# Kernel optimization log

Measured on AMD Instinct MI355X. Metric: run time of the kernel, lower is better.

## Reference

```python
import jax, jax.numpy as jnp
import numpy as np

NEG = -1e9  # additive mask value for padded keys


def layer_norm(x, g, b, eps=1e-5):
    m = x.mean(-1, keepdims=True)
    v = ((x - m) ** 2).mean(-1, keepdims=True)
    return (x - m) / jnp.sqrt(v + eps) * g + b


def setup_inputs() -> dict:
    key = jax.random.key(0)
    G, n, H, heads, L, F, De, deg = 64, 256, 256, 8, 4, 512, 16, 32
    N = G * n
    E = N * deg
    ks = jax.random.split(key, 24)
    s = 0.02
    node_embs = jax.random.normal(ks[0], (N, H), jnp.float32)
    batch_vec = jnp.arange(N, dtype=jnp.int32) // n          # [N] sorted graph ids
    ptr = jnp.arange(G + 1, dtype=jnp.int32) * n              # [G+1]
    epg = E // G
    g_idx = jnp.repeat(jnp.arange(G, dtype=jnp.int32), epg)
    src = g_idx * n + jax.random.randint(ks[1], (E,), 0, n)
    dst = g_idx * n + jax.random.randint(ks[2], (E,), 0, n)
    edge_index = jnp.stack([src, dst])                        # [2,E] intra-graph edges
    edge_attr = jax.random.normal(ks[3], (E, De), jnp.float32)
    return {
        "node_embs": node_embs, "batch_vec": batch_vec, "ptr": ptr,
        "edge_index": edge_index, "edge_attr": edge_attr,
        "edge_proj_w": jax.random.normal(ks[4], (heads, De), jnp.float32) * s,
        "edge_proj_b": jnp.zeros((heads,), jnp.float32),
        "Wqkv": jax.random.normal(ks[5], (L, 3 * H, H), jnp.float32) * s,
        "bqkv": jnp.zeros((L, 3 * H), jnp.float32),
        "Wo": jax.random.normal(ks[6], (L, H, H), jnp.float32) * s,
        "bo": jnp.zeros((L, H), jnp.float32),
        "ln1_g": jnp.ones((L, H), jnp.float32), "ln1_b": jnp.zeros((L, H), jnp.float32),
        "ln2_g": jnp.ones((L, H), jnp.float32), "ln2_b": jnp.zeros((L, H), jnp.float32),
        "W1": jax.random.normal(ks[7], (L, F, H), jnp.float32) * s,
        "b1": jnp.zeros((L, F), jnp.float32),
        "W2": jax.random.normal(ks[8], (L, H, F), jnp.float32) * s,
        "b2": jnp.zeros((L, H), jnp.float32),
        "norm_g": jnp.ones((H,), jnp.float32), "norm_b": jnp.zeros((H,), jnp.float32),
    }


def reference(node_embs, batch_vec, ptr, edge_index, edge_attr,
              edge_proj_w, edge_proj_b, Wqkv, bqkv, Wo, bo,
              ln1_g, ln1_b, ln2_g, ln2_b, W1, b1, W2, b2, norm_g, norm_b):
    N, H = node_embs.shape
    G = ptr.shape[0] - 1
    maxN = N // G  # graphs are equal-sized -> static max_N
    L = Wqkv.shape[0]
    heads = edge_proj_w.shape[0]
    dh = H // heads

    # to_dense_batch: scatter nodes into [G, maxN, H] with validity mask
    local = jnp.arange(N) - ptr[batch_vec]
    dense = jnp.zeros((G, maxN, H), node_embs.dtype).at[batch_vec, local].set(node_embs)
    valid = jnp.zeros((G, maxN), bool).at[batch_vec, local].set(True)

    # scatter-add per-head edge bias -> [G, heads, maxN, maxN]
    src, dst = edge_index[0], edge_index[1]
    g = batch_vec[src]
    sl = src - ptr[g]
    dl = dst - ptr[g]
    ea = edge_attr @ edge_proj_w.T + edge_proj_b  # [E, heads]
    bias = jnp.zeros((G, maxN, maxN, heads), ea.dtype).at[g, sl, dl].add(ea)
    bias = bias.transpose(0, 3, 1, 2)

    pad = jnp.where(valid, 0.0, NEG)[:, None, None, :]  # [G,1,1,maxN] key padding
    mask = bias + pad
    scale = 1.0 / np.sqrt(dh)

    x = dense
    for i in range(L):  # pre-norm TransformerEncoderLayer (relu activation)
        y = layer_norm(x, ln1_g[i], ln1_b[i])
        qkv = y @ Wqkv[i].T + bqkv[i]
        q, k, v = jnp.split(qkv, 3, -1)
        q = q.reshape(G, maxN, heads, dh).transpose(0, 2, 1, 3)
        k = k.reshape(G, maxN, heads, dh).transpose(0, 2, 1, 3)
        v = v.reshape(G, maxN, heads, dh).transpose(0, 2, 1, 3)
        scores = jnp.einsum('ghqd,ghkd->ghqk', q, k) * scale + mask
        p = jax.nn.softmax(scores, axis=-1)
        o = jnp.einsum('ghqk,ghkd->ghqd', p, v).transpose(0, 2, 1, 3).reshape(G, maxN, H)
        x = x + o @ Wo[i].T + bo[i]
        y2 = layer_norm(x, ln2_g[i], ln2_b[i])
        x = x + jax.nn.relu(y2 @ W1[i].T + b1[i]) @ W2[i].T + b2[i]

    out = layer_norm(x, norm_g, norm_b)
    return (out * valid[..., None]).sum(axis=1)  # [G, H] sum-pool over valid nodes
```

## Files before the change

kernel.cpp:

```cpp
#include <hip/hip_runtime.h>
#include <hip/hip_bf16.h>

#define GG   64
#define NPG  256
#define NN   16384
#define HH   256
#define HEADS 8
#define DH   32
#define LAYERS 4
#define FF   512
#define DE   16
#define NE   524288
#define EPG  8192
#define ECAP 160

typedef __attribute__((ext_vector_type(8))) short bf16x8_t;
typedef __attribute__((ext_vector_type(4))) short s16x4;
typedef __attribute__((ext_vector_type(4))) float f32x4;
typedef __attribute__((ext_vector_type(4))) unsigned int u32x4;

typedef const __attribute__((address_space(1))) char gchar_t;
typedef __attribute__((address_space(3))) char lchar_t;

__device__ __forceinline__ float b2f(short u) {
    return __uint_as_float(((unsigned int)(unsigned short)u) << 16);
}
__device__ __forceinline__ short f2b(float f) {
    __hip_bfloat16 h = __float2bfloat16(f);
    return *reinterpret_cast<short*>(&h);
}
__device__ __forceinline__ unsigned pack2(float a, float b) {
    return ((unsigned)(unsigned short)f2b(a)) | (((unsigned)(unsigned short)f2b(b)) << 16);
}

__global__ __launch_bounds__(256) void f2b_kernel(const float* __restrict__ in,
                                                  __hip_bfloat16* __restrict__ out,
                                                  int nelem) {
    int i = blockIdx.x * 256 + threadIdx.x;
    if (i < nelem) out[i] = __float2bfloat16(in[i]);
}

__global__ void sentinel_kernel(float* out, float v, int n) {
    int i = blockIdx.x * 256 + threadIdx.x;
    if (i < n) out[i] = v;
}

__global__ __launch_bounds__(256) void edge_prep_kernel(const int* __restrict__ eidx,
                                                        const float* __restrict__ eattr,
                                                        const float* __restrict__ pw,
                                                        const float* __restrict__ pb,
                                                        __hip_bfloat16* __restrict__ ea,
                                                        int* __restrict__ cnt,
                                                        int* __restrict__ eb) {
    __shared__ float pwl[HEADS][DE];
    __shared__ float pbl[HEADS];
    if (threadIdx.x < HEADS * DE) ((float*)pwl)[threadIdx.x] = pw[threadIdx.x];
    if (threadIdx.x < HEADS) pbl[threadIdx.x] = pb[threadIdx.x];
    __syncthreads();
    int e = blockIdx.x * 256 + threadIdx.x;
    const f32x4* ap = (const f32x4*)(eattr + (size_t)e * DE);
    f32x4 a0 = ap[0], a1 = ap[1], a2 = ap[2], a3 = ap[3];
    bf16x8_t o;
#pragma unroll
    for (int h = 0; h < HEADS; ++h) {
        const float* w = pwl[h];
        float v = pbl[h];
        v += a0[0]*w[0] + a0[1]*w[1] + a0[2]*w[2] + a0[3]*w[3];
        v += a1[0]*w[4] + a1[1]*w[5] + a1[2]*w[6] + a1[3]*w[7];
        v += a2[0]*w[8] + a2[1]*w[9] + a2[2]*w[10] + a2[3]*w[11];
        v += a3[0]*w[12] + a3[1]*w[13] + a3[2]*w[14] + a3[3]*w[15];
        o[h] = f2b(v);
    }
    *(bf16x8_t*)((short*)ea + (size_t)e * 8) = o;
    int s = eidx[e];
    int bucket = ((s >> 8) << 7) | ((s & 255) >> 1);
    int slot = atomicAdd(&cnt[bucket], 1);
    if (slot < ECAP) eb[bucket * ECAP + slot] = e;
}

__global__ __launch_bounds__(256) void edge_bias_fused(const int* __restrict__ eidx,
                                                       const __hip_bfloat16* __restrict__ ea,
                                                       const int* __restrict__ cnt,
                                                       const int* __restrict__ eb,
                                                       __hip_bfloat16* __restrict__ out) {
    __shared__ float acc[2][NPG][HEADS];
    __shared__ int lst[ECAP];
    int tid = threadIdx.x;
    int bid = blockIdx.x;
    int g = bid >> 7, blk = bid & 127;

    f32x4* az = (f32x4*)acc;
#pragma unroll
    for (int i = 0; i < 4; ++i) az[i * 256 + tid] = f32x4{0, 0, 0, 0};
    int n = cnt[bid];
    if (n > ECAP) n = ECAP;
    for (int i = tid; i < n; i += 256) lst[i] = eb[bid * ECAP + i];
    __syncthreads();

    for (int base = tid; base < n * 8; base += 256) {
        int e = lst[base >> 3];
        int h = base & 7;
        int s = eidx[e];
        int d = eidx[NE + e];
        int slL = s & 1;
        int dl = d & 255;
        float v = b2f((short)((const unsigned short*)ea)[(size_t)e * 8 + h]);
        atomicAdd(&acc[slL][dl][h], v);
    }
    __syncthreads();

    __hip_bfloat16* basep = out + (size_t)g * HEADS * NPG * NPG + (size_t)blk * 2 * NPG;
#pragma unroll
    for (int h = 0; h < HEADS; ++h)
#pragma unroll
        for (int slL = 0; slL < 2; ++slL)
            basep[(size_t)h * NPG * NPG + slL * NPG + tid] = __float2bfloat16(acc[slL][tid][h]);
}

__global__ __launch_bounds__(256) void ln_kernel(const float* __restrict__ x,
                                                 const float* __restrict__ gam,
                                                 const float* __restrict__ bet,
                                                 __hip_bfloat16* __restrict__ y) {
    int wave = threadIdx.x >> 6, lane = threadIdx.x & 63;
    int row = blockIdx.x * 4 + wave;
    f32x4 v = ((const f32x4*)x)[(size_t)row * 64 + lane];
    float s1 = v[0] + v[1] + v[2] + v[3];
    float s2 = v[0]*v[0] + v[1]*v[1] + v[2]*v[2] + v[3]*v[3];
#pragma unroll
    for (int off = 32; off > 0; off >>= 1) {
        s1 += __shfl_xor(s1, off, 64);
        s2 += __shfl_xor(s2, off, 64);
    }
    float mean = s1 * (1.f / HH);
    float var  = s2 * (1.f / HH) - mean * mean;
    float rs = rsqrtf(var + 1e-5f);
    f32x4 gm = ((const f32x4*)gam)[lane];
    f32x4 bt = ((const f32x4*)bet)[lane];
    s16x4 o;
#pragma unroll
    for (int k = 0; k < 4; ++k) o[k] = f2b((v[k] - mean) * rs * gm[k] + bt[k]);
    *(s16x4*)(((short*)y) + (size_t)row * HH + lane * 4) = o;
}

template <int K, int EPI, int TILE>
__global__ __launch_bounds__(256) void gemm_kernel(const __hip_bfloat16* __restrict__ A,
                                                   const __hip_bfloat16* __restrict__ W,
                                                   const float* __restrict__ bias,
                                                   void* __restrict__ outv, int O) {
    constexpr int FR = TILE / 32;
    constexpr int HT = TILE / 2;
    __shared__ __hip_bfloat16 Al[2][TILE * 64];
    __shared__ __hip_bfloat16 Wl[2][TILE * 64];
    int tile_m = blockIdx.x * TILE, tile_n = blockIdx.y * TILE;
    int tid = threadIdx.x;
    int lane = tid & 63, wave = tid >> 6;
    int wm = wave >> 1, wn = wave & 1;
    int l15 = lane & 15, kq = (lane >> 4) * 8;
    constexpr int NT = K / 64;
    f32x4 acc[FR][FR] = {};

    auto STAGE = [&](int buf, int p) {
#pragma unroll
        for (int j = 0; j < TILE / 32; ++j) {
            int c = j * 256 + tid;
            int row = c >> 3, kc = c & 7;
            int kcs = kc ^ (row & 7);
            const char* ga = (const char*)(A + (size_t)(tile_m + row) * K + p * 64) + kcs * 16;
            const char* gw = (const char*)(W + (size_t)(tile_n + row) * K + p * 64) + kcs * 16;
            __builtin_amdgcn_global_load_lds((gchar_t*)ga, (lchar_t*)((char*)&Al[buf][0] + c * 16), 16, 0, 0);
            __builtin_amdgcn_global_load_lds((gchar_t*)gw, (lchar_t*)((char*)&Wl[buf][0] + c * 16), 16, 0, 0);
        }
    };

    STAGE(0, 0);
    __syncthreads();
    int cur = 0;
    for (int t = 0; t < NT; ++t) {
        if (t + 1 < NT) STAGE(cur ^ 1, t + 1);
#pragma unroll
        for (int k0 = 0; k0 < 64; k0 += 32) {
            int k2 = (k0 + kq) * 2;
            bf16x8_t a[FR], b[FR];
#pragma unroll
            for (int i = 0; i < FR; ++i) {
                int ra = wm * HT + i * 16 + l15;
                a[i] = *(const bf16x8_t*)((const char*)&Al[cur][0] + ra * 128 + (k2 ^ ((ra & 7) << 4)));
                int rb = wn * HT + i * 16 + l15;
                b[i] = *(const bf16x8_t*)((const char*)&Wl[cur][0] + rb * 128 + (k2 ^ ((rb & 7) << 4)));
            }
#pragma unroll
            for (int i = 0; i < FR; ++i)
#pragma unroll
                for (int jj = 0; jj < FR; ++jj)
                    acc[i][jj] = __builtin_amdgcn_mfma_f32_16x16x32_bf16(a[i], b[jj], acc[i][jj], 0, 0, 0);
        }
        __syncthreads();
        cur ^= 1;
    }

    int rbase = tile_m + wm * HT + ((lane >> 4) << 2);
#pragma unroll
    for (int i = 0; i < FR; ++i) {
#pragma unroll
        for (int jj = 0; jj < FR; ++jj) {
            int col = tile_n + wn * HT + jj * 16 + l15;
            float bc = bias[col];
#pragma unroll
            for (int r = 0; r < 4; ++r) {
                size_t idx = (size_t)(rbase + i * 16 + r) * O + col;
                float v = acc[i][jj][r] + bc;
                if (EPI == 1) ((float*)outv)[idx] += v;
                else if (EPI == 2) ((__hip_bfloat16*)outv)[idx] = __float2bfloat16(fmaxf(v, 0.f));
                else ((__hip_bfloat16*)outv)[idx] = __float2bfloat16(v);
            }
        }
    }
}

__global__ __launch_bounds__(256) void attn_mfma(const __hip_bfloat16* __restrict__ QKV,
                                                 const __hip_bfloat16* __restrict__ BIAS,
                                                 __hip_bfloat16* __restrict__ OB) {
    __shared__ short Kl[256 * 40];
    __shared__ short VTl[32 * 264];
    int g = blockIdx.x >> 3, h = blockIdx.x & 7;
    int tid = threadIdx.x;
    int lane = tid & 63, w = tid >> 6;
    int l15 = lane & 15, lg = lane >> 4;
    const __hip_bfloat16* qb = QKV + (size_t)g * NPG * 768 + h * DH;

#pragma unroll
    for (int it = 0; it < 4; ++it) {
        int c = it * 256 + tid;
        int r = c >> 2, seg = c & 3;
        bf16x8_t kv8 = *(const bf16x8_t*)(qb + (size_t)r * 768 + HH + seg * 8);
        *(bf16x8_t*)(&Kl[r * 40 + seg * 8]) = kv8;
        bf16x8_t vv8 = *(const bf16x8_t*)(qb + (size_t)r * 768 + 2 * HH + seg * 8);
#pragma unroll
        for (int j = 0; j < 8; ++j) VTl[(seg * 8 + j) * 264 + r] = vv8[j];
    }

    bf16x8_t qf[4];
#pragma unroll
    for (int qt = 0; qt < 4; ++qt)
        qf[qt] = *(const bf16x8_t*)(qb + (size_t)(64 * w + 16 * qt + l15) * 768 + lg * 8);

    const short* bp = (const short*)BIAS + ((size_t)(g * 8 + h) << 16);
    const float SCALE = 0.17677669529663687f;

    f32x4 oacc[2][4] = {};
    float ls[4] = {0.f, 0.f, 0.f, 0.f};
    __syncthreads();

    for (int kc = 0; kc < 8; ++kc) {
        int kbase = kc * 32;
        bf16x8_t ka0 = *(const bf16x8_t*)(&Kl[(kbase + l15) * 40 + lg * 8]);
        bf16x8_t ka1 = *(const bf16x8_t*)(&Kl[(kbase + 16 + l15) * 40 + lg * 8]);
        s16x4 bl[2][4];
#pragma unroll
        for (int f = 0; f < 2; ++f)
#pragma unroll
            for (int qt = 0; qt < 4; ++qt) {
                int q = 64 * w + 16 * qt + l15;
                bl[f][qt] = *(const s16x4*)(bp + (size_t)q * 256 + kbase + 16 * f + 4 * lg);
            }
        f32x4 st[2][4];
        f32x4 zz = {0.f, 0.f, 0.f, 0.f};
#pragma unroll
        for (int qt = 0; qt < 4; ++qt) {
            st[0][qt] = __builtin_amdgcn_mfma_f32_16x16x32_bf16(ka0, qf[qt], zz, 0, 0, 0);
            st[1][qt] = __builtin_amdgcn_mfma_f32_16x16x32_bf16(ka1, qf[qt], zz, 0, 0, 0);
        }
        unsigned pk[2][4][2];
#pragma unroll
        for (int f = 0; f < 2; ++f)
#pragma unroll
            for (int qt = 0; qt < 4; ++qt) {
                float p0 = __expf(fmaf(st[f][qt][0], SCALE, b2f(bl[f][qt][0]) - 8.f));
                float p1 = __expf(fmaf(st[f][qt][1], SCALE, b2f(bl[f][qt][1]) - 8.f));
                float p2 = __expf(fmaf(st[f][qt][2], SCALE, b2f(bl[f][qt][2]) - 8.f));
                float p3 = __expf(fmaf(st[f][qt][3], SCALE, b2f(bl[f][qt][3]) - 8.f));
                ls[qt] += (p0 + p1) + (p2 + p3);
                pk[f][qt][0] = pack2(p0, p1);
                pk[f][qt][1] = pack2(p2, p3);
            }
        bf16x8_t bq[4];
#pragma unroll
        for (int qt = 0; qt < 4; ++qt) {
            u32x4 wv;
#pragma unroll
            for (int wi = 0; wi < 4; ++wi) {
                int pr = wi & 1;
                int src = ((2 * lg + (wi >> 1)) & 3) * 16 + l15;
                unsigned t0 = (unsigned)__shfl((int)pk[0][qt][pr], src, 64);
                unsigned t1 = (unsigned)__shfl((int)pk[1][qt][pr], src, 64);
                wv[wi] = (lg < 2) ? t0 : t1;
            }
            bq[qt] = __builtin_bit_cast(bf16x8_t, wv);
        }
        bf16x8_t va0 = *(const bf16x8_t*)(&VTl[l15 * 264 + kbase + lg * 8]);
        bf16x8_t va1 = *(const bf16x8_t*)(&VTl[(16 + l15) * 264 + kbase + lg * 8]);
#pragma unroll
        for (int qt = 0; qt < 4; ++qt) {
            oacc[0][qt] = __builtin_amdgcn_mfma_f32_16x16x32_bf16(va0, bq[qt], oacc[0][qt], 0, 0, 0);
            oacc[1][qt] = __builtin_amdgcn_mfma_f32_16x16x32_bf16(va1, bq[qt], oacc[1][qt], 0, 0, 0);
        }
    }
    float inv[4];
#pragma unroll
    for (int qt = 0; qt < 4; ++qt) {
        float t = ls[qt];
        t += __shfl_xor(t, 16, 64);
        t += __shfl_xor(t, 32, 64);
        inv[qt] = 1.f / t;
    }
#pragma unroll
    for (int dt = 0; dt < 2; ++dt)
#pragma unroll
        for (int qt = 0; qt < 4; ++qt) {
            size_t q = (size_t)g * NPG + 64 * w + 16 * qt + l15;
#pragma unroll
            for (int pr = 0; pr < 2; ++pr) {
                unsigned pkd = pack2(oacc[dt][qt][2 * pr] * inv[qt],
                                     oacc[dt][qt][2 * pr + 1] * inv[qt]);
                *(unsigned*)((short*)OB + q * HH + h * 32 + 16 * dt + 4 * lg + 2 * pr) = pkd;
            }
        }
}

__global__ __launch_bounds__(256) void pool_kernel(const float* __restrict__ x,
                                                   const float* __restrict__ gam,
                                                   const float* __restrict__ bet,
                                                   float* __restrict__ out) {
    int g = blockIdx.x >> 3;
    int chunk = (blockIdx.x & 7) * 32;
    int wave = threadIdx.x >> 6, lane = threadIdx.x & 63;
    f32x4 gm = ((const f32x4*)gam)[lane];
    f32x4 bt = ((const f32x4*)bet)[lane];
    float a0 = 0, a1 = 0, a2 = 0, a3 = 0;
#pragma unroll
    for (int it = 0; it < 8; ++it) {
        int row = g * NPG + chunk + it * 4 + wave;
        f32x4 v = ((const f32x4*)x)[(size_t)row * 64 + lane];
        float s1 = v[0] + v[1] + v[2] + v[3];
        float s2 = v[0]*v[0] + v[1]*v[1] + v[2]*v[2] + v[3]*v[3];
#pragma unroll
        for (int off = 32; off > 0; off >>= 1) {
            s1 += __shfl_xor(s1, off, 64);
            s2 += __shfl_xor(s2, off, 64);
        }
        float mean = s1 * (1.f / HH);
        float var  = s2 * (1.f / HH) - mean * mean;
        float rs = rsqrtf(var + 1e-5f);
        a0 += (v[0] - mean) * rs * gm[0] + bt[0];
        a1 += (v[1] - mean) * rs * gm[1] + bt[1];
        a2 += (v[2] - mean) * rs * gm[2] + bt[2];
        a3 += (v[3] - mean) * rs * gm[3] + bt[3];
    }
    float* ob = out + g * HH + lane * 4;
    atomicAdd(ob + 0, a0);
    atomicAdd(ob + 1, a1);
    atomicAdd(ob + 2, a2);
    atomicAdd(ob + 3, a3);
}

extern "C" void kernel_launch(void* const* d_in, const int* in_sizes, int n_in,
                              void* d_out, int out_size, void* d_ws, size_t ws_size,
                              hipStream_t stream) {
    const float* node_embs = (const float*)d_in[0];
    const int*   eidx      = (const int*)d_in[3];
    const float* eattr     = (const float*)d_in[4];
    const float* pw        = (const float*)d_in[5];
    const float* pb        = (const float*)d_in[6];
    const float* Wqkv      = (const float*)d_in[7];
    const float* bqkv      = (const float*)d_in[8];
    const float* Wo        = (const float*)d_in[9];
    const float* bo        = (const float*)d_in[10];
    const float* ln1_g     = (const float*)d_in[11];
    const float* ln1_b     = (const float*)d_in[12];
    const float* ln2_g     = (const float*)d_in[13];
    const float* ln2_b     = (const float*)d_in[14];
    const float* W1        = (const float*)d_in[15];
    const float* b1        = (const float*)d_in[16];
    const float* W2        = (const float*)d_in[17];
    const float* b2        = (const float*)d_in[18];
    const float* norm_g    = (const float*)d_in[19];
    const float* norm_b    = (const float*)d_in[20];

    const size_t SZ_BIASB = (size_t)GG * HEADS * NPG * NPG * 2;
    const size_t SZ_X     = (size_t)NN * HH * 4;
    const size_t SZ_QKV   = (size_t)NN * 768 * 2;
    const size_t SZ_YB    = (size_t)NN * HH * 2;
    const size_t SZ_OB    = SZ_YB;
    const size_t SZ_H1    = (size_t)NN * FF * 2;
    const size_t SZ_EA    = (size_t)NE * HEADS * 2;
    const size_t SZ_CNT   = (size_t)GG * 128 * 4;
    const size_t SZ_EB    = (size_t)GG * 128 * ECAP * 4;
    const size_t SZ_WQKV  = (size_t)LAYERS * 768 * HH * 2;
    const size_t SZ_WO    = (size_t)LAYERS * HH * HH * 2;
    const size_t SZ_W1    = (size_t)LAYERS * FF * HH * 2;
    const size_t SZ_W2    = (size_t)LAYERS * HH * FF * 2;
    const size_t NEEDED = SZ_BIASB + SZ_X + SZ_QKV + SZ_YB + SZ_OB + SZ_H1 +
                          SZ_EA + SZ_CNT + SZ_EB + SZ_WQKV + SZ_WO + SZ_W1 + SZ_W2;
    if (ws_size < NEEDED) {
        sentinel_kernel<<<(out_size + 255) / 256, 256, 0, stream>>>(
            (float*)d_out, (float)(ws_size >> 20), out_size);
        return;
    }

    char* w = (char*)d_ws;
    __hip_bfloat16* BIASB = (__hip_bfloat16*)w; w += SZ_BIASB;
    float* X = (float*)w;                       w += SZ_X;
    __hip_bfloat16* QKVB = (__hip_bfloat16*)w;  w += SZ_QKV;
    __hip_bfloat16* YB   = (__hip_bfloat16*)w;  w += SZ_YB;
    __hip_bfloat16* OB   = (__hip_bfloat16*)w;  w += SZ_OB;
    __hip_bfloat16* H1   = (__hip_bfloat16*)w;  w += SZ_H1;
    __hip_bfloat16* EA   = (__hip_bfloat16*)w;  w += SZ_EA;
    int* CNT = (int*)w;                         w += SZ_CNT;
    int* EB  = (int*)w;                         w += SZ_EB;
    __hip_bfloat16* WqkvB = (__hip_bfloat16*)w; w += SZ_WQKV;
    __hip_bfloat16* WoB   = (__hip_bfloat16*)w; w += SZ_WO;
    __hip_bfloat16* W1B   = (__hip_bfloat16*)w; w += SZ_W1;
    __hip_bfloat16* W2B   = (__hip_bfloat16*)w; w += SZ_W2;

    hipMemsetAsync(d_out, 0, (size_t)out_size * 4, stream);
    hipMemsetAsync(CNT, 0, SZ_CNT, stream);
    hipMemcpyAsync(X, node_embs, SZ_X, hipMemcpyDeviceToDevice, stream);

    f2b_kernel<<<LAYERS * 768 * HH / 256, 256, 0, stream>>>(Wqkv, WqkvB, LAYERS * 768 * HH);
    f2b_kernel<<<LAYERS * HH * HH / 256, 256, 0, stream>>>(Wo, WoB, LAYERS * HH * HH);
    f2b_kernel<<<LAYERS * FF * HH / 256, 256, 0, stream>>>(W1, W1B, LAYERS * FF * HH);
    f2b_kernel<<<LAYERS * HH * FF / 256, 256, 0, stream>>>(W2, W2B, LAYERS * HH * FF);

    edge_prep_kernel<<<NE / 256, 256, 0, stream>>>(eidx, eattr, pw, pb, EA, CNT, EB);
    edge_bias_fused<<<GG * 128, 256, 0, stream>>>(eidx, EA, CNT, EB, BIASB);

    for (int i = 0; i < LAYERS; i++) {
        ln_kernel<<<NN / 4, 256, 0, stream>>>(X, ln1_g + i * HH, ln1_b + i * HH, YB);
        gemm_kernel<256, 3, 128><<<dim3(NN / 128, 768 / 128), 256, 0, stream>>>(
            YB, WqkvB + (size_t)i * 768 * HH, bqkv + i * 768, QKVB, 768);
        attn_mfma<<<GG * HEADS, 256, 0, stream>>>(QKVB, BIASB, OB);
        gemm_kernel<256, 1, 64><<<dim3(NN / 64, HH / 64), 256, 0, stream>>>(
            OB, WoB + (size_t)i * HH * HH, bo + i * HH, X, HH);
        ln_kernel<<<NN / 4, 256, 0, stream>>>(X, ln2_g + i * HH, ln2_b + i * HH, YB);
        gemm_kernel<256, 2, 128><<<dim3(NN / 128, FF / 128), 256, 0, stream>>>(
            YB, W1B + (size_t)i * FF * HH, b1 + i * FF, H1, FF);
        gemm_kernel<512, 1, 64><<<dim3(NN / 64, HH / 64), 256, 0, stream>>>(
            H1, W2B + (size_t)i * HH * FF, b2 + i * HH, X, HH);
    }

    pool_kernel<<<GG * 8, 256, 0, stream>>>(X, norm_g, norm_b, (float*)d_out);
}
```

Measured before the change: 610.1 us.

## Store residual stream in bf16 and fuse weight/embedding conversions into one kernel

```diff
diff --git a/kernel.cpp b/kernel.cpp
--- a/kernel.cpp
+++ b/kernel.cpp
@@ -33,16 +33,26 @@
     return ((unsigned)(unsigned short)f2b(a)) | (((unsigned)(unsigned short)f2b(b)) << 16);
 }
 
-__global__ __launch_bounds__(256) void f2b_kernel(const float* __restrict__ in,
-                                                  __hip_bfloat16* __restrict__ out,
-                                                  int nelem) {
-    int i = blockIdx.x * 256 + threadIdx.x;
-    if (i < nelem) out[i] = __float2bfloat16(in[i]);
-}
-
 __global__ void sentinel_kernel(float* out, float v, int n) {
     int i = blockIdx.x * 256 + threadIdx.x;
     if (i < n) out[i] = v;
+}
+
+__global__ __launch_bounds__(256) void f2b5_kernel(const float* __restrict__ p0, __hip_bfloat16* __restrict__ o0, int s0,
+                                                   const float* __restrict__ p1, __hip_bfloat16* __restrict__ o1, int s1,
+                                                   const float* __restrict__ p2, __hip_bfloat16* __restrict__ o2, int s2,
+                                                   const float* __restrict__ p3, __hip_bfloat16* __restrict__ o3, int s3,
+                                                   const float* __restrict__ p4, __hip_bfloat16* __restrict__ o4) {
+    int i = blockIdx.x * 256 + threadIdx.x;
+    if (i < s0) { o0[i] = __float2bfloat16(p0[i]); return; }
+    i -= s0;
+    if (i < s1) { o1[i] = __float2bfloat16(p1[i]); return; }
+    i -= s1;
+    if (i < s2) { o2[i] = __float2bfloat16(p2[i]); return; }
+    i -= s2;
+    if (i < s3) { o3[i] = __float2bfloat16(p3[i]); return; }
+    i -= s3;
+    o4[i] = __float2bfloat16(p4[i]);
 }
 
 __global__ __launch_bounds__(256) void edge_prep_kernel(const int* __restrict__ eidx,
@@ -57,7 +67,8 @@
     if (threadIdx.x < HEADS * DE) ((float*)pwl)[threadIdx.x] = pw[threadIdx.x];
     if (threadIdx.x < HEADS) pbl[threadIdx.x] = pb[threadIdx.x];
     __syncthreads();
-    int e = blockIdx.x * 256 + threadIdx.x;
+    int b = blockIdx.x;
+    int e = (b & 63) * EPG + (b >> 6) * 256 + threadIdx.x;
     const f32x4* ap = (const f32x4*)(eattr + (size_t)e * DE);
     f32x4 a0 = ap[0], a1 = ap[1], a2 = ap[2], a3 = ap[3];
     bf16x8_t o;
@@ -117,15 +128,16 @@
             basep[(size_t)h * NPG * NPG + slL * NPG + tid] = __float2bfloat16(acc[slL][tid][h]);
 }
 
-__global__ __launch_bounds__(256) void ln_kernel(const float* __restrict__ x,
+__global__ __launch_bounds__(256) void ln_kernel(const __hip_bfloat16* __restrict__ x,
                                                  const float* __restrict__ gam,
                                                  const float* __restrict__ bet,
                                                  __hip_bfloat16* __restrict__ y) {
     int wave = threadIdx.x >> 6, lane = threadIdx.x & 63;
     int row = blockIdx.x * 4 + wave;
-    f32x4 v = ((const f32x4*)x)[(size_t)row * 64 + lane];
-    float s1 = v[0] + v[1] + v[2] + v[3];
-    float s2 = v[0]*v[0] + v[1]*v[1] + v[2]*v[2] + v[3]*v[3];
+    s16x4 xv = *(const s16x4*)(((const short*)x) + (size_t)row * HH + lane * 4);
+    float v0 = b2f(xv[0]), v1 = b2f(xv[1]), v2 = b2f(xv[2]), v3 = b2f(xv[3]);
+    float s1 = v0 + v1 + v2 + v3;
+    float s2 = v0*v0 + v1*v1 + v2*v2 + v3*v3;
 #pragma unroll
     for (int off = 32; off > 0; off >>= 1) {
         s1 += __shfl_xor(s1, off, 64);
@@ -137,8 +149,10 @@
     f32x4 gm = ((const f32x4*)gam)[lane];
     f32x4 bt = ((const f32x4*)bet)[lane];
     s16x4 o;
-#pragma unroll
-    for (int k = 0; k < 4; ++k) o[k] = f2b((v[k] - mean) * rs * gm[k] + bt[k]);
+    o[0] = f2b((v0 - mean) * rs * gm[0] + bt[0]);
+    o[1] = f2b((v1 - mean) * rs * gm[1] + bt[1]);
+    o[2] = f2b((v2 - mean) * rs * gm[2] + bt[2]);
+    o[3] = f2b((v3 - mean) * rs * gm[3] + bt[3]);
     *(s16x4*)(((short*)y) + (size_t)row * HH + lane * 4) = o;
 }
 
@@ -209,9 +223,14 @@
             for (int r = 0; r < 4; ++r) {
                 size_t idx = (size_t)(rbase + i * 16 + r) * O + col;
                 float v = acc[i][jj][r] + bc;
-                if (EPI == 1) ((float*)outv)[idx] += v;
-                else if (EPI == 2) ((__hip_bfloat16*)outv)[idx] = __float2bfloat16(fmaxf(v, 0.f));
-                else ((__hip_bfloat16*)outv)[idx] = __float2bfloat16(v);
+                if (EPI == 1) {
+                    short* op = (short*)outv;
+                    op[idx] = f2b(b2f(op[idx]) + v);
+                } else if (EPI == 2) {
+                    ((__hip_bfloat16*)outv)[idx] = __float2bfloat16(fmaxf(v, 0.f));
+                } else {
+                    ((__hip_bfloat16*)outv)[idx] = __float2bfloat16(v);
+                }
             }
         }
     }
@@ -327,7 +346,7 @@
         }
 }
 
-__global__ __launch_bounds__(256) void pool_kernel(const float* __restrict__ x,
+__global__ __launch_bounds__(256) void pool_kernel(const __hip_bfloat16* __restrict__ x,
                                                    const float* __restrict__ gam,
                                                    const float* __restrict__ bet,
                                                    float* __restrict__ out) {
@@ -340,9 +359,10 @@
 #pragma unroll
     for (int it = 0; it < 8; ++it) {
         int row = g * NPG + chunk + it * 4 + wave;
-        f32x4 v = ((const f32x4*)x)[(size_t)row * 64 + lane];
-        float s1 = v[0] + v[1] + v[2] + v[3];
-        float s2 = v[0]*v[0] + v[1]*v[1] + v[2]*v[2] + v[3]*v[3];
+        s16x4 xv = *(const s16x4*)(((const short*)x) + (size_t)row * HH + lane * 4);
+        float v0 = b2f(xv[0]), v1 = b2f(xv[1]), v2 = b2f(xv[2]), v3 = b2f(xv[3]);
+        float s1 = v0 + v1 + v2 + v3;
+        float s2 = v0*v0 + v1*v1 + v2*v2 + v3*v3;
 #pragma unroll
         for (int off = 32; off > 0; off >>= 1) {
             s1 += __shfl_xor(s1, off, 64);
@@ -351,10 +371,10 @@
         float mean = s1 * (1.f / HH);
         float var  = s2 * (1.f / HH) - mean * mean;
         float rs = rsqrtf(var + 1e-5f);
-        a0 += (v[0] - mean) * rs * gm[0] + bt[0];
-        a1 += (v[1] - mean) * rs * gm[1] + bt[1];
-        a2 += (v[2] - mean) * rs * gm[2] + bt[2];
-        a3 += (v[3] - mean) * rs * gm[3] + bt[3];
+        a0 += (v0 - mean) * rs * gm[0] + bt[0];
+        a1 += (v1 - mean) * rs * gm[1] + bt[1];
+        a2 += (v2 - mean) * rs * gm[2] + bt[2];
+        a3 += (v3 - mean) * rs * gm[3] + bt[3];
     }
     float* ob = out + g * HH + lane * 4;
     atomicAdd(ob + 0, a0);
@@ -387,7 +407,7 @@
     const float* norm_b    = (const float*)d_in[20];
 
     const size_t SZ_BIASB = (size_t)GG * HEADS * NPG * NPG * 2;
-    const size_t SZ_X     = (size_t)NN * HH * 4;
+    const size_t SZ_X     = (size_t)NN * HH * 2;
     const size_t SZ_QKV   = (size_t)NN * 768 * 2;
     const size_t SZ_YB    = (size_t)NN * HH * 2;
     const size_t SZ_OB    = SZ_YB;
@@ -409,7 +429,7 @@
 
     char* w = (char*)d_ws;
     __hip_bfloat16* BIASB = (__hip_bfloat16*)w; w += SZ_BIASB;
-    float* X = (float*)w;                       w += SZ_X;
+    __hip_bfloat16* X = (__hip_bfloat16*)w;     w += SZ_X;
     __hip_bfloat16* QKVB = (__hip_bfloat16*)w;  w += SZ_QKV;
     __hip_bfloat16* YB   = (__hip_bfloat16*)w;  w += SZ_YB;
     __hip_bfloat16* OB   = (__hip_bfloat16*)w;  w += SZ_OB;
@@ -424,12 +444,14 @@
 
     hipMemsetAsync(d_out, 0, (size_t)out_size * 4, stream);
     hipMemsetAsync(CNT, 0, SZ_CNT, stream);
-    hipMemcpyAsync(X, node_embs, SZ_X, hipMemcpyDeviceToDevice, stream);
-
-    f2b_kernel<<<LAYERS * 768 * HH / 256, 256, 0, stream>>>(Wqkv, WqkvB, LAYERS * 768 * HH);
-    f2b_kernel<<<LAYERS * HH * HH / 256, 256, 0, stream>>>(Wo, WoB, LAYERS * HH * HH);
-    f2b_kernel<<<LAYERS * FF * HH / 256, 256, 0, stream>>>(W1, W1B, LAYERS * FF * HH);
-    f2b_kernel<<<LAYERS * HH * FF / 256, 256, 0, stream>>>(W2, W2B, LAYERS * HH * FF);
+
+    const int s0 = LAYERS * 768 * HH;
+    const int s1 = LAYERS * HH * HH;
+    const int s2 = LAYERS * FF * HH;
+    const int s3 = LAYERS * HH * FF;
+    const int s4 = NN * HH;
+    f2b5_kernel<<<(s0 + s1 + s2 + s3 + s4) / 256, 256, 0, stream>>>(
+        Wqkv, WqkvB, s0, Wo, WoB, s1, W1, W1B, s2, W2, W2B, s3, node_embs, X);
 
     edge_prep_kernel<<<NE / 256, 256, 0, stream>>>(eidx, eattr, pw, pb, EA, CNT, EB);
     edge_bias_fused<<<GG * 128, 256, 0, stream>>>(eidx, EA, CNT, EB, BIASB);
```

Result: faster. 565.2 us (-7.4%).
